# Kernel tuning notes

Measured on AMD Instinct MI355X. Metric: run time of the kernel, lower is better.

The kernel has to match this reference:

```python
import jax, jax.numpy as jnp
import numpy as np
from jax import lax

N = 200; E = 3200; HID = 64; NH = 16; OUT = 2 * HID; CAT = NH * OUT  # CAT = 2048
ALPHA = 0.2


def _gat(h, e_attr, adj, n2n, W, a_s, a_d, a_e, We, concat):
    # edge-feature-aware GAT head: logits from Wh_i, Wh_j and projected node2node feats
    Nn = h.shape[0]
    Wh = h @ W                                       # [N, out]
    ee = ((n2n @ We) @ a_e).reshape(Nn, Nn)          # [N, N] edge-feature term
    logits = jax.nn.leaky_relu((Wh @ a_s)[:, None] + (Wh @ a_d)[None, :] + ee,
                               negative_slope=ALPHA)
    logits = jnp.where(adj > 0, logits, -1e9)        # mask to graph structure
    att = jax.nn.softmax(logits, axis=1)
    h2 = att @ Wh
    if concat:
        h2 = jax.nn.elu(h2)
    return h2, jax.nn.elu(e_attr @ We)               # updated node + edge features


def _edge_pool(x, eidx, e, w, b):
    # static-shape edge pooling: score edges, gate nodes by mean incident score
    src, dst = eidx[0], eidx[1]
    s = jax.nn.sigmoid(jnp.concatenate([x[src], x[dst], e], axis=1) @ w + b)  # [E]
    deg = jax.ops.segment_sum(jnp.ones_like(s), src, num_segments=x.shape[0])
    ns = jax.ops.segment_sum(s, src, num_segments=x.shape[0]) / (deg + 1e-6)
    return x * ns[:, None], e * s[:, None]


def _gpool(x, w, b):
    # GlobalAttention: gate_nn = Linear+Sigmoid, softmax over nodes, weighted sum
    gate = jax.nn.softmax(jax.nn.sigmoid(x @ w + b), axis=0)  # [N, 1]
    return jnp.sum(gate * x, axis=0, keepdims=True)           # [1, D]


def _adj_n2n(Nn, eidx, eattr):
    # vectorized version of the per-edge Python loop in _get_adj_node2node
    src, dst = eidx[0], eidx[1]
    adj = jnp.zeros((Nn, Nn), eattr.dtype).at[src, dst].set(1.0)
    n2n = jnp.zeros((Nn * Nn, eattr.shape[1]), eattr.dtype).at[src * Nn + dst].set(eattr)
    return adj, n2n


def _lstm_dir(x, Wih, Whh, b):
    # one LSTM direction over seq x [T, Din] (PyTorch i,f,g,o gate order)
    Hh = Whh.shape[1]
    def step(carry, xt):
        h, c = carry
        g = xt @ Wih.T + h @ Whh.T + b
        i, f, gg, o = jnp.split(g, 4)
        c = jax.nn.sigmoid(f) * c + jax.nn.sigmoid(i) * jnp.tanh(gg)
        h = jax.nn.sigmoid(o) * jnp.tanh(c)
        return (h, c), h
    (_, _), ys = lax.scan(step, (jnp.zeros(Hh, x.dtype), jnp.zeros(Hh, x.dtype)), x)
    return ys


def setup_inputs():
    key = jax.random.key(0)
    ks = iter(jax.random.split(key, 64))
    def rn(shape, scale=0.05):
        return jax.random.normal(next(ks), shape, jnp.float32) * scale
    inp = {}
    for g in (1, 2):
        eidx = jax.random.randint(next(ks), (2, E), 0, N)
        eattr = rn((E, HID), 1.0)
        adj, n2n = _adj_n2n(N, eidx, eattr)
        inp['features%d' % g] = rn((N, HID), 1.0)
        inp['edge_index%d' % g] = eidx
        inp['edgesAttr%d' % g] = eattr
        inp['adjacency%d' % g] = adj
        inp['node2node%d' % g] = n2n
    inp.update(dict(
        W_h=rn((HID, HID)),
        W_gat=rn((NH, HID, OUT)), a_src=rn((NH, OUT)), a_dst=rn((NH, OUT)),
        a_e=rn((NH, OUT)), We_gat=rn((NH, HID, OUT)),
        W_out=rn((CAT, OUT)), ao_src=rn((OUT,)), ao_dst=rn((OUT,)), ao_e=rn((OUT,)),
        We_out=rn((CAT, OUT)),
        ep1_w=rn((3 * CAT,)), ep1_b=rn(()),
        ep2_w=rn((3 * OUT,)), ep2_b=rn(()),
        g1_w=rn((HID, 1)), g1_b=rn((1,)),
        g2_w=rn((CAT, 1)), g2_b=rn((1,)),
        g3_w=rn((OUT, 1)), g3_b=rn((1,)),
        Wih0=rn((2, 512, 35 * HID)), Whh0=rn((2, 512, 128)), b0=rn((2, 512)),
        Wih1=rn((2, 512, 256)), Whh1=rn((2, 512, 128)), b1=rn((2, 512)),
        fc_w=rn((256, 2)), fc_b=rn((2,)),
    ))
    return inp


def reference(features1, features2, edge_index1, edge_index2, edgesAttr1, edgesAttr2,
              adjacency1, adjacency2, node2node1, node2node2,
              W_h, W_gat, a_src, a_dst, a_e, We_gat,
              W_out, ao_src, ao_dst, ao_e, We_out,
              ep1_w, ep1_b, ep2_w, ep2_b,
              g1_w, g1_b, g2_w, g2_b, g3_w, g3_b,
              Wih0, Whh0, b0, Wih1, Whh1, b1, fc_w, fc_b):
    def graph(feat, eidx, eattr, adj, n2n):
        h = jax.nn.elu(feat @ W_h)                              # SingleNodeAttentionLayer
        hs = [_gpool(h, g1_w, g1_b)]
        outs = [_gat(h, eattr, adj, n2n, W_gat[i], a_src[i], a_dst[i], a_e[i],
                     We_gat[i], True) for i in range(NH)]
        h = jnp.concatenate([o[0] for o in outs], axis=1)       # [N, 2048]
        eattr = jnp.concatenate([o[1] for o in outs], axis=1)   # [E, 2048]
        h, eattr = _edge_pool(h, eidx, eattr, ep1_w, ep1_b)
        hs.append(_gpool(h, g2_w, g2_b))
        adj2, n2n2 = _adj_n2n(h.shape[0], eidx, eattr)          # dense [N*N, 2048]
        h, eattr = _gat(h, eattr, adj2, n2n2, W_out, ao_src, ao_dst, ao_e, We_out, False)
        h, eattr = _edge_pool(h, eidx, eattr, ep2_w, ep2_b)
        hs.append(_gpool(h, g3_w, g3_b))
        return jnp.concatenate(hs, axis=1)                      # [1, 35*HID]

    h1 = graph(features1, edge_index1, edgesAttr1, adjacency1, node2node1)
    h2 = graph(features2, edge_index2, edgesAttr2, adjacency2, node2node2)
    x = jnp.concatenate([h1, h2], axis=0)                       # seq [2, 2240]
    for Wih, Whh, b in ((Wih0, Whh0, b0), (Wih1, Whh1, b1)):
        f = _lstm_dir(x, Wih[0], Whh[0], b[0])
        r = _lstm_dir(x[::-1], Wih[1], Whh[1], b[1])[::-1]
        x = jnp.concatenate([f, r], axis=1)                     # [2, 256]
    logits = x[-1] @ fc_w + fc_b
    return jax.nn.softmax(logits)[None, :]                      # [1, nclass]
```

## Files before the change

kernel.cpp:

```cpp
#include <hip/hip_runtime.h>
#include <math.h>

#define DI static __device__ __forceinline__

DI float eluf(float x){ return x > 0.f ? x : expm1f(x); }
DI float lreluf(float x){ return x > 0.f ? x : 0.2f*x; }
DI float sigmf(float x){ return 1.f/(1.f+expf(-x)); }

typedef unsigned short u16;
typedef unsigned int   u32;
typedef __attribute__((ext_vector_type(8))) short short8_t;
typedef __attribute__((ext_vector_type(4))) float f32x4;

DI u16 bf16rne(float f){
  u32 u = __float_as_uint(f);
  u += 0x7fffu + ((u>>16)&1u);
  return (u16)(u>>16);
}

DI f32x4 bmfma(short8_t a, short8_t b, f32x4 c){
  return __builtin_amdgcn_mfma_f32_16x16x32_bf16(a, b, c, 0, 0, 0);
}

constexpr int N=200, E=3200, HID=64, NH=16, OUTD=128, CAT=2048, SEQD=2240;
// ... 55 lines not shown
  const float *ep1_w, *ep1_b, *ep2_w, *ep2_b;
  const float *g1_w, *g1_b, *g2_w, *g2_b, *g3_w, *g3_b;
  const float *Wih0, *Whh0, *b0, *Wih1, *Whh1, *b1, *fc_w, *fc_b;
  float *out;
};

constexpr int ZPG  = 2*E + 1024;
constexpr int IB_Z = (2*ZPG+255)/256;
constexpr int IB_C = (2*N*N+255)/256;
constexpr int IB_D = (2*2*512*128)/256;
constexpr int IB_E = (NH*HID+CAT+3)/4;
constexpr int IB_H = (2*N+3)/4;
constexpr int IB_W1 = (NH*OUTD*HID)/256;
constexpr int IB_W2 = (OUTD*CAT)/256;
constexpr int IB_EA = (2*E*HID)/256;
__global__ void k_init(Params P){
  int b = blockIdx.x, tid = threadIdx.x;
  if (b < IB_Z){
    int i = b*256 + tid;
    if (i < 2*ZPG){
      int g = i/ZPG, r = i%ZPG;
      int addr = r<E ? OEW1+r : (r<2*E ? OEWV+(r-E) :
                 (r<2*E+512 ? ODEG1+(r-2*E) : ODEG2+(r-2*E-512)));
      gf(g)[addr] = 0.f;
    }
  } else if (b < IB_Z+IB_C){
    int i = (b-IB_Z)*256 + tid; if (i < 2*N*N) G_PIDX[i] = -1;
  } else if (b < IB_Z+IB_C+IB_D){
    int idx = (b-IB_Z-IB_C)*256 + tid;
    int l = idx >> 17;
    int r = idx & 131071;
    int d = r >> 16;
    int r2 = r & 65535;
    int gate = r2 & 511;
    int k = r2 >> 9;
    const float* Whh = l ? P.Whh1 : P.Whh0;
    G_WHHT[idx] = Whh[((size_t)d*512+gate)*128 + k];
  } else if (b < IB_Z+IB_C+IB_D+IB_E){
    int gid = (b-IB_Z-IB_C-IB_D)*4 + (tid>>6);
    int lane = tid & 63;
    if (gid < NH*HID){
      int h = gid/HID, c = gid%HID;
      const float* W = P.We_gat + (size_t)(h*HID+c)*OUTD;
      const float* a = P.a_e + h*OUTD;
      float acc = 0.f;
      for (int o=lane;o<OUTD;o+=64) acc += W[o]*a[o];
      for (int off=32;off>0;off>>=1) acc += __shfl_down(acc,off);
      if (lane==0) gwe_ae()[gid] = acc;
    } else if (gid < NH*HID+CAT){
      int c = gid - NH*HID;
      const float* W = P.We_out + (size_t)c*OUTD;
      float acc = 0.f;
      for (int o=lane;o<OUTD;o+=64) acc += W[o]*P.ao_e[o];
      for (int off=32;off>0;off>>=1) acc += __shfl_down(acc,off);
      if (lane==0) gv_e()[c] = acc;
    }
  } else if (b < IB_Z+IB_C+IB_D+IB_E+IB_H){
    int unit = (b-IB_Z-IB_C-IB_D-IB_E)*4 + (tid>>6);
    if (unit >= 2*N) return;
    int g = unit / N, n = unit % N, c = tid & 63;
    const float* feat = P.g[g].feat;
    float acc = 0.f;
    for (int k=0;k<HID;k++) acc += feat[n*HID+k]*P.W_h[k*HID+c];
    float v = eluf(acc);
    float* f = gf(g);
    f[OH0 + n*HID + c] = v;
    float r = v*P.g1_w[c];
    for (int off=32;off>0;off>>=1) r += __shfl_down(r,off);
    if (c==0) f[ORAW1+n] = r;
  } else if (b < IB_Z+IB_C+IB_D+IB_E+IB_H+IB_W1){
    int i = (b-(IB_Z+IB_C+IB_D+IB_E+IB_H))*256 + tid;
    int h = i>>13, o = (i>>6)&127, c = i&63;
    G_WGAT_T[i] = bf16rne(P.We_gat[(size_t)(h*HID+c)*OUTD + o]);
  } else if (b < IB_Z+IB_C+IB_D+IB_E+IB_H+IB_W1+IB_W2){
    int i = (b-(IB_Z+IB_C+IB_D+IB_E+IB_H+IB_W1))*256 + tid;
    int n = i>>11, q = i&2047;
    G_WOUT_T[i] = bf16rne(P.We_out[(size_t)q*OUTD + n]);
  } else {
    int i = (b-(IB_Z+IB_C+IB_D+IB_E+IB_H+IB_W1+IB_W2))*256 + tid;
    int g = i >= E*HID ? 1 : 0;
    G_EATTR_BF[i] = bf16rne(P.g[g].eattr[i - g*E*HID]);
  }
}

__global__ void k_edoth(Params P){
  int b = blockIdx.x, tid = threadIdx.x;
  int g = b / (E/16);
  int e0 = (b % (E/16)) * 16;
  __shared__ float ea[16][HID+1];
  __shared__ float wa[16][HID+1];
  {
    int row = tid >> 4, c0 = (tid & 15)*4;
    float4 v = *(const float4*)&P.g[g].eattr[(size_t)(e0+row)*HID + c0];
    ea[row][c0]=v.x; ea[row][c0+1]=v.y; ea[row][c0+2]=v.z; ea[row][c0+3]=v.w;
    float4 w = *(const float4*)&gwe_ae()[row*HID + c0];
    wa[row][c0]=w.x; wa[row][c0+1]=w.y; wa[row][c0+2]=w.z; wa[row][c0+3]=w.w;
  }
  __syncthreads();
  int h = tid >> 4, el = tid & 15;
  float acc = 0.f;
  #pragma unroll
  for (int c=0;c<HID;c++) acc += ea[el][c]*wa[h][c];
  G_EDOTH[((size_t)g*NH + h)*E + e0 + el] = acc;
}

__global__ void k_Wh(Params P){
  int n = blockIdx.x, h = blockIdx.y, g = blockIdx.z, o = threadIdx.x;
  float* f = gf(g);
  if (h == NH){
    if (n != 0) return;
    __shared__ float att[N];
    __shared__ float sb[128];
    for (int j = o; j < N; j += 128) att[j] = sigmf(f[ORAW1+j] + P.g1_b[0]);
    __syncthreads();
    float m = -3e38f;
    for (int j = o; j < N; j += 128) m = fmaxf(m, att[j]);
    sb[o] = m; __syncthreads();
    for (int s=64;s>0;s>>=1){ if (o<s) sb[o]=fmaxf(sb[o],sb[o+s]); __syncthreads(); }
    m = sb[0]; __syncthreads();
    float ss = 0.f;
    for (int j = o; j < N; j += 128){ float e = expf(att[j]-m); ss += e; }
    sb[o] = ss; __syncthreads();
    for (int s=64;s>0;s>>=1){ if (o<s) sb[o]+=sb[o+s]; __syncthreads(); }
    float inv = 1.f/sb[0]; __syncthreads();
    for (int j = o; j < N; j += 128) att[j] = expf(att[j]-m)*inv;
    __syncthreads();
    if (o < HID){
      float acc = 0.f;
      for (int j=0;j<N;j++) acc += att[j]*f[OH0 + j*HID + o];
      gxseq()[g*SEQD + o] = acc;
    }
    return;
  }
  __shared__ float hs[HID];
  __shared__ float sred[128], dred[128];
  if (o < HID) hs[o] = f[OH0 + n*HID + o];
  __syncthreads();
  const float* W = P.W_gat + (size_t)h*HID*OUTD + o;
  float acc = 0.f;
  for (int c=0;c<HID;c++) acc += hs[c]*W[(size_t)c*OUTD];
  f[OWH + ((size_t)h*N + n)*OUTD + o] = acc;
  sred[o] = acc*P.a_src[h*OUTD+o];
  dred[o] = acc*P.a_dst[h*OUTD+o];
  __syncthreads();
  for (int s=64;s>0;s>>=1){ if (o<s){ sred[o]+=sred[o+s]; dred[o]+=dred[o+s]; } __syncthreads(); }
  if (o==0){ f[OASN+h*N+n]=sred[0]; f[OADN+h*N+n]=dred[0]; }
}

__global__ void k_att1(Params P){
  int nb = blockIdx.x, h = blockIdx.y, g = blockIdx.z, tid = threadIdx.x;
  int n0 = nb*4;
  __shared__ float z[4][N];
  __shared__ float red[128];
  __shared__ float sinv[4];
  float* f = gf(g);
  const float* adj = P.g[g].adj;
  const int* pidx = gpidx(g);
  const float* edoth = G_EDOTH + ((size_t)g*NH + h)*E;
  const float* adn = f + OADN + h*N;
  for (int i=0;i<4;i++){
    float asn = f[OASN + h*N + n0+i];
    for (int j = tid; j < N; j += 128){
      float a = adj[(n0+i)*N + j];
      float zz;
      if (a > 0.f){
        int p = pidx[(n0+i)*N + j];
        float ee = (p >= 0) ? edoth[p] : 0.f;
        zz = lreluf(asn + adn[j] + ee);
      } else zz = -1e9f;
      z[i][j] = zz;
    }
  }
  __syncthreads();
  for (int i=0;i<4;i++){
    float m = -3e38f;
    for (int j = tid; j < N; j += 128) m = fmaxf(m, z[i][j]);
    red[tid] = m; __syncthreads();
    for (int s=64;s>0;s>>=1){ if (tid<s) red[tid]=fmaxf(red[tid],red[tid+s]); __syncthreads(); }
    m = red[0]; __syncthreads();
    float ssum = 0.f;
    for (int j = tid; j < N; j += 128){ float e = expf(z[i][j]-m); z[i][j]=e; ssum += e; }
    red[tid] = ssum; __syncthreads();
    for (int s=64;s>0;s>>=1){ if (tid<s) red[tid]+=red[tid+s]; __syncthreads(); }
    if (tid==0) sinv[i] = 1.f/red[0];
    __syncthreads();
  }
  const float* wh = f + OWH + (size_t)h*N*OUTD;
  float a0=0.f,a1=0.f,a2=0.f,a3=0.f;
  for (int j=0;j<N;j++){
    float w = wh[(size_t)j*OUTD + tid];
    a0 += z[0][j]*w; a1 += z[1][j]*w; a2 += z[2][j]*w; a3 += z[3][j]*w;
  }
  f[OH1 + (size_t)(n0+0)*CAT + h*OUTD + tid] = eluf(a0*sinv[0]);
  f[OH1 + (size_t)(n0+1)*CAT + h*OUTD + tid] = eluf(a1*sinv[1]);
  f[OH1 + (size_t)(n0+2)*CAT + h*OUTD + tid] = eluf(a2*sinv[2]);
  f[OH1 + (size_t)(n0+3)*CAT + h*OUTD + tid] = eluf(a3*sinv[3]);
}

__global__ void k_xw1(Params P){
  int n = blockIdx.x, g = blockIdx.y, tid = threadIdx.x;
  __shared__ float s1b[256], s2b[256], s3b[256];
  float* f = gf(g);
  const float* x = f + OH1 + (size_t)n*CAT;
  float a1 = 0.f, a2 = 0.f, a3 = 0.f;
  for (int c = tid; c < CAT; c += 256){
    float xv = x[c];
    a1 += xv*P.ep1_w[c];
    a2 += xv*P.ep1_w[CAT+c];
    a3 += xv*P.g2_w[c];
  }
  s1b[tid]=a1; s2b[tid]=a2; s3b[tid]=a3; __syncthreads();
  for (int s=128;s>0;s>>=1){
    if (tid<s){ s1b[tid]+=s1b[tid+s]; s2b[tid]+=s2b[tid+s]; s3b[tid]+=s3b[tid+s]; }
    __syncthreads();
  }
  if (tid==0){ f[OXW1+n]=s1b[0]; f[OXW2+n]=s2b[0]; f[ORAW2+n]=s3b[0]; }
}

__global__ void k_s1(Params P){
  int e = blockIdx.x*256 + threadIdx.x, g = blockIdx.y;
  if (e >= E) return;
  float* f = gf(g);
  const int* ei = P.g[g].eidx;
  int s = ei[e], d = ei[E+e];
  float v = sigmf(f[OXW1+s] + f[OXW2+d] + f[OEW1+e] + P.ep1_b[0]);
  f[OS1+e] = v;
  atomicAdd(&f[OSS1+s], v);
  atomicAdd(&f[ODEG1+s], 1.f);
}

__global__ void k_pairs(Params P){
  int e = blockIdx.x*256 + threadIdx.x, g = blockIdx.y;
  if (e >= E) return;
  const int* ei = P.g[g].eidx;
  atomicMax(&gpidx(g)[ei[e]*N + ei[E+e]], e);
}

__global__ void k_gpool_out(Params P, int xoff, int D, int odeg, int rawoff,
                            const float* b, int outoff){
  int cb = blockIdx.x, g = blockIdx.y, tid = threadIdx.x;
  __shared__ float att[N];
  __shared__ float sb[256];
  float* f = gf(g);
  for (int n = tid; n < N; n += 256){
    float sc = f[odeg+256+n]/(f[odeg+n]+1e-6f);
    att[n] = sigmf(f[rawoff+n]*sc + b[0]);
  }
  __syncthreads();
  float m = -3e38f;
  for (int n = tid; n < N; n += 256) m = fmaxf(m, att[n]);
  sb[tid] = m; __syncthreads();
  for (int s=128;s>0;s>>=1){ if (tid<s) sb[tid]=fmaxf(sb[tid],sb[tid+s]); __syncthreads(); }
  m = sb[0]; __syncthreads();
  float ss = 0.f;
  for (int n = tid; n < N; n += 256){ float e = expf(att[n]-m); ss += e; }
  sb[tid] = ss; __syncthreads();
  for (int s=128;s>0;s>>=1){ if (tid<s) sb[tid]+=sb[tid+s]; __syncthreads(); }
  float inv = 1.f/sb[0]; __syncthreads();
  for (int n = tid; n < N; n += 256){
    float sc = f[odeg+256+n]/(f[odeg+n]+1e-6f);
    att[n] = expf(att[n]-m)*inv*sc;
  }
  __syncthreads();
  int c = cb*256 + tid;
  if (c < D){
    const float* x = f + xoff;
    float acc = 0.f;
    for (int n=0;n<N;n++) acc += att[n]*x[(size_t)n*D + c];
    gxseq()[g*SEQD + outoff + c] = acc;
  }
}

__global__ void k_Wh2(Params P){
  int n = blockIdx.x, g = blockIdx.y, tid = threadIdx.x;
  int kq = tid >> 7, o = tid & 127;
  __shared__ float hrow[4][128];
  __shared__ float part[4][128];
  __shared__ float sr[128], dr[128];
  float* f = gf(g);
  const float* x = f + OH1 + (size_t)n*CAT;
  float acc = 0.f;
  for (int cc=0; cc<4; cc++){
    int c0 = kq*512 + cc*128;
    __syncthreads();
    hrow[kq][o] = x[c0 + o];
    __syncthreads();
    const float* W = P.W_out + (size_t)c0*OUTD + o;
    for (int j=0;j<128;j++) acc += hrow[kq][j]*W[(size_t)j*OUTD];
  }
  part[kq][o] = acc;
  __syncthreads();
  if (kq==0){
    float ns = f[OSS1+n]/(f[ODEG1+n]+1e-6f);
    float a = part[0][o]+part[1][o]+part[2][o]+part[3][o];
    float v = a*ns;
    f[OWH2 + (size_t)n*OUTD + o] = v;
    sr[o] = v*P.ao_src[o];
    dr[o] = v*P.ao_dst[o];
  }
  __syncthreads();
  for (int s=64;s>0;s>>=1){
    if (tid<s){ sr[tid]+=sr[tid+s]; dr[tid]+=dr[tid+s]; }
    __syncthreads();
  }
  if (tid==0){ f[OAS2+n]=sr[0]; f[OAD2+n]=dr[0]; }
}

__global__ void k_att2(Params P){
  int n = blockIdx.x, g = blockIdx.y, tid = threadIdx.x;
  __shared__ float z[N];
  __shared__ float red[128];
  __shared__ float dred[128];
  __shared__ float gred[128];
  float* f = gf(g);
  const float* adj = P.g[g].adj;
  const int* pidx = gpidx(g);
  float asn = f[OAS2+n];
  const float* adn = f + OAD2;
  for (int j = tid; j < N; j += 128){
    float a = adj[n*N + j];
    float zz;
    if (a > 0.f){
      int p = pidx[n*N + j];
      float ee = (p >= 0) ? f[OEWV+p]*f[OS1+p] : 0.f;
      zz = lreluf(asn + adn[j] + ee);
    } else zz = -1e9f;
    z[j] = zz;
  }
  __syncthreads();
  float m = -3e38f;
  for (int j = tid; j < N; j += 128) m = fmaxf(m, z[j]);
  red[tid] = m; __syncthreads();
  for (int s=64;s>0;s>>=1){ if (tid<s) red[tid]=fmaxf(red[tid],red[tid+s]); __syncthreads(); }
  m = red[0]; __syncthreads();
  float ssum = 0.f;
  for (int j = tid; j < N; j += 128){ float e = expf(z[j]-m); z[j]=e; ssum += e; }
  red[tid] = ssum; __syncthreads();
  for (int s=64;s>0;s>>=1){ if (tid<s) red[tid]+=red[tid+s]; __syncthreads(); }
  float inv = 1.f/red[0]; __syncthreads();
  const float* wh = f + OWH2;
  float acc = 0.f;
  for (int j=0;j<N;j++){
    float w = z[j];
    if (w != 0.f) acc += w * wh[(size_t)j*OUTD + tid];
  }
  float v = acc*inv;
  f[OH2B + (size_t)n*OUTD + tid] = v;
  red[tid]  = v*P.ep2_w[tid];
  dred[tid] = v*P.ep2_w[OUTD+tid];
  gred[tid] = v*P.g3_w[tid];
  __syncthreads();
  for (int s=64;s>0;s>>=1){
    if (tid<s){ red[tid]+=red[tid+s]; dred[tid]+=dred[tid+s]; gred[tid]+=gred[tid+s]; }
    __syncthreads();
  }
  if (tid==0){ f[OXS2+n]=red[0]; f[OXD2+n]=dred[0]; f[ORAW3+n]=gred[0]; }
}

__global__ __launch_bounds__(256) void k_e2p_mfma(Params P){
  int eb = blockIdx.x, hg = blockIdx.y, g = blockIdx.z;
  int tid = threadIdx.x;
  int wave = tid>>6, lane = tid&63, l16 = lane&15, l4 = lane>>4;
  __shared__ __attribute__((aligned(16))) u16 Tlds[32*512];
  int e0 = eb*32;
  int nt0 = wave*2;
  const u16* ea = G_EATTR_BF + ((size_t)g*E + e0)*HID;
  short8_t af00 = *(const short8_t*)(ea + l16*HID + l4*8);
  short8_t af01 = *(const short8_t*)(ea + l16*HID + 32 + l4*8);
  short8_t af10 = *(const short8_t*)(ea + (16+l16)*HID + l4*8);
  short8_t af11 = *(const short8_t*)(ea + (16+l16)*HID + 32 + l4*8);
  float ew1p0[4] = {0.f,0.f,0.f,0.f}, ewvp0[4] = {0.f,0.f,0.f,0.f};
  float ew1p1[4] = {0.f,0.f,0.f,0.f}, ewvp1[4] = {0.f,0.f,0.f,0.f};
  for (int hh=0; hh<4; hh++){
    int h = hg*4 + hh;
    const u16* Wg = G_WGAT_T + (size_t)h*OUTD*HID;
    #pragma unroll
    for (int nn=0; nn<2; nn++){
      int nt = nt0 + nn;
      const u16* Wgn = Wg + (size_t)(nt*16 + l16)*HID + l4*8;
      short8_t wg0 = *(const short8_t*)Wgn;
      short8_t wg1 = *(const short8_t*)(Wgn + 32);
      f32x4 d0 = {0.f,0.f,0.f,0.f}, d1 = {0.f,0.f,0.f,0.f};
      d0 = bmfma(af00, wg0, d0);
      d1 = bmfma(af10, wg0, d1);
      d0 = bmfma(af01, wg1, d0);
      d1 = bmfma(af11, wg1, d1);
      int qg = h*OUTD + nt*16 + l16;
      float w1 = P.ep1_w[2*CAT + qg];
      float wv = gv_e()[qg];
      int qloc = hh*128 + nt*16 + l16;
      #pragma unroll
      for (int r=0;r<4;r++){
        float v0 = d0[r] > 0.f ? d0[r] : expm1f(d0[r]);
        float v1 = d1[r] > 0.f ? d1[r] : expm1f(d1[r]);
        ew1p0[r] += v0*w1; ewvp0[r] += v0*wv;
        ew1p1[r] += v1*w1; ewvp1[r] += v1*wv;
        int row = l4*4 + r;
        int byt = (row*1024 + qloc*2) ^ ((row&7)<<4);
        *(u16*)((char*)Tlds + byt) = bf16rne(v0);
        *(u16*)((char*)Tlds + byt + 16384) = bf16rne(v1);
      }
    }
  }
  const u16* WoA = G_WOUT_T + (size_t)(wave*32 + l16)*CAT + hg*512 + l4*8;
  const u16* WoB = WoA + 16*CAT;
  short8_t w0a = *(const short8_t*)WoA;
  short8_t w0b = *(const short8_t*)WoB;
  short8_t w1a = *(const short8_t*)(WoA + 32);
  short8_t w1b = *(const short8_t*)(WoB + 32);
  float* f = gf(g);
  #pragma unroll
  for (int r=0;r<4;r++){
    float a0 = ew1p0[r], b0 = ewvp0[r], a1 = ew1p1[r], b1 = ewvp1[r];
    a0 += __shfl_xor(a0,1); b0 += __shfl_xor(b0,1); a1 += __shfl_xor(a1,1); b1 += __shfl_xor(b1,1);
    a0 += __shfl_xor(a0,2); b0 += __shfl_xor(b0,2); a1 += __shfl_xor(a1,2); b1 += __shfl_xor(b1,2);
    a0 += __shfl_xor(a0,4); b0 += __shfl_xor(b0,4); a1 += __shfl_xor(a1,4); b1 += __shfl_xor(b1,4);
    a0 += __shfl_xor(a0,8); b0 += __shfl_xor(b0,8); a1 += __shfl_xor(a1,8); b1 += __shfl_xor(b1,8);
    if (l16==0){
      int e = e0 + l4*4 + r;
      atomicAdd(&f[OEW1+e], a0);
      atomicAdd(&f[OEWV+e], b0);
      atomicAdd(&f[OEW1+e+16], a1);
      atomicAdd(&f[OEWV+e+16], b1);
    }
  }
  __syncthreads();
  f32x4 acc00 = {0.f,0.f,0.f,0.f}, acc01 = {0.f,0.f,0.f,0.f};
  f32x4 acc10 = {0.f,0.f,0.f,0.f}, acc11 = {0.f,0.f,0.f,0.f};
  #pragma unroll
  for (int ks=0; ks<16; ks++){
    short8_t na = w0a, nb = w0b;
    if (ks < 14){
      na = *(const short8_t*)(WoA + (ks+2)*32);
      nb = *(const short8_t*)(WoB + (ks+2)*32);
    }
    int byt = (l16*1024 + ks*64 + l4*16) ^ ((l16&7)<<4);
    short8_t a0 = *(const short8_t*)((const char*)Tlds + byt);
    short8_t a1 = *(const short8_t*)((const char*)Tlds + byt + 16384);
    acc00 = bmfma(a0, w0a, acc00);
    acc10 = bmfma(a1, w0a, acc10);
    acc01 = bmfma(a0, w0b, acc01);
    acc11 = bmfma(a1, w0b, acc11);
    w0a = w1a; w0b = w1b; w1a = na; w1b = nb;
  }
  float* dst = G_E2PART + (((size_t)hg*2 + g)*E + e0)*OUTD;
  #pragma unroll
  for (int r=0;r<4;r++){
    int ee = l4*4 + r;
    dst[(size_t)ee*OUTD + wave*32 + l16]      = acc00[r];
    dst[(size_t)ee*OUTD + wave*32 + 16 + l16] = acc01[r];
    dst[(size_t)(16+ee)*OUTD + wave*32 + l16]      = acc10[r];
    dst[(size_t)(16+ee)*OUTD + wave*32 + 16 + l16] = acc11[r];
  }
}

constexpr int TE2 = 16;
__global__ void k_ew2fin(Params P){
  int e0 = blockIdx.x*TE2, g = blockIdx.y, tid = threadIdx.x;
  __shared__ float lred[2][TE2];
  float* f = gf(g);
  float w2 = P.ep2_w[2*OUTD + tid];
  int lane = tid & 63, wvi = tid >> 6;
  for (int e=0;e<TE2;e++){
    const float* src = G_E2PART + ((size_t)g*E + e0 + e)*OUTD + tid;
    float a = 0.f;
    for (int h=0;h<4;h++) a += src[(size_t)h*2*E*OUTD];
    float v = eluf(f[OS1+e0+e]*a) * w2;
    for (int off=32;off>0;off>>=1) v += __shfl_down(v,off);
    if (lane==0) lred[wvi][e]=v;
  }
  __syncthreads();
  if (tid < TE2){
    int e = e0 + tid;
    float ew2 = lred[0][tid]+lred[1][tid];
    const int* ei = P.g[g].eidx;
    int s = ei[e], d = ei[E+e];
    float v = sigmf(f[OXS2+s] + f[OXD2+d] + ew2 + P.ep2_b[0]);
    atomicAdd(&f[OSS2+s], v);
    atomicAdd(&f[ODEG2+s], 1.f);
  }
}

__global__ void k_lstm_xg(Params P, int layer){
  int gid = blockIdx.x*4 + (threadIdx.x>>6);
  int lane = threadIdx.x & 63;
  int t = gid >> 10;
  int rem = gid & 1023;
  int d = rem >> 9;
  int gate = rem & 511;
  const float* Wih = layer ? P.Wih1 : P.Wih0;
  const float* bb  = layer ? P.b1   : P.b0;
  const float* xin = layer ? gy0()  : gxseq();
  int Din = layer ? 256 : SEQD;
  const float* x = xin + t*Din;
  const float* Wr = Wih + ((size_t)d*512 + gate)*Din;
  float acc = 0.f;
  for (int k=lane; k<Din; k+=64) acc += x[k]*Wr[k];
  for (int off=32; off>0; off>>=1) acc += __shfl_down(acc, off);
  if (lane==0) gxg()[(t*2 + d)*512 + gate] = acc + bb[d*512 + gate];
}

__global__ void k_lstm_rec(Params P, int layer){
  int d = blockIdx.x, tid = threadIdx.x;
  float* yout = layer ? gy1() : gy0();
  const float* T = G_WHHT + (size_t)(layer*2 + d)*128*512;
  __shared__ float h[128], c[128], gbuf[512];
  if (tid < 128){ h[tid]=0.f; c[tid]=0.f; }
  __syncthreads();
  for (int s=0;s<2;s++){
    int t = (d==0) ? s : 1-s;
    float acc = gxg()[(t*2 + d)*512 + tid];
    for (int k=0;k<128;k++) acc += h[k]*T[(size_t)k*512 + tid];
    gbuf[tid] = acc;
    __syncthreads();
    if (tid < 128){
      float ii = sigmf(gbuf[tid]);
      float ff = sigmf(gbuf[128+tid]);
      float gg = tanhf(gbuf[256+tid]);
      float oo = sigmf(gbuf[384+tid]);
      float cn = ff*c[tid] + ii*gg;
      c[tid] = cn;
      float hn = oo*tanhf(cn);
      h[tid] = hn;
      yout[t*256 + d*128 + tid] = hn;
    }
    __syncthreads();
  }
}

__global__ void k_final(Params P){
  int tid = threadIdx.x;
  __shared__ float sb[256], sb2[256];
  const float* x = gy1() + 256;
  sb[tid]  = x[tid]*P.fc_w[tid*2+0];
  sb2[tid] = x[tid]*P.fc_w[tid*2+1];
  __syncthreads();
  for (int s=128;s>0;s>>=1){ if (tid<s){ sb[tid]+=sb[tid+s]; sb2[tid]+=sb2[tid+s]; } __syncthreads(); }
  if (tid==0){
    float l0 = sb[0] + P.fc_b[0];
    float l1 = sb2[0] + P.fc_b[1];
    float m = fmaxf(l0,l1);
    float e0 = expf(l0-m), e1 = expf(l1-m), inv = 1.f/(e0+e1);
    P.out[0] = e0*inv;
    P.out[1] = e1*inv;
  }
}

extern "C" void kernel_launch(void* const* d_in, const int* in_sizes, int n_in,
                              void* d_out, int out_size, void* d_ws, size_t ws_size,
                              hipStream_t stream){
  Params P;
  for (int g=0; g<2; ++g){
    int b = g*5;
    P.g[g].feat  = (const float*)d_in[b+0];
    P.g[g].eidx  = (const int*)d_in[b+1];
    P.g[g].eattr = (const float*)d_in[b+2];
    P.g[g].adj   = (const float*)d_in[b+3];
    P.g[g].n2n   = (const float*)d_in[b+4];
  }
  P.W_h   = (const float*)d_in[10];
  P.W_gat = (const float*)d_in[11];
  P.a_src = (const float*)d_in[12];
  P.a_dst = (const float*)d_in[13];
  P.a_e   = (const float*)d_in[14];
  P.We_gat= (const float*)d_in[15];
  P.W_out = (const float*)d_in[16];
  P.ao_src= (const float*)d_in[17];
  P.ao_dst= (const float*)d_in[18];
  P.ao_e  = (const float*)d_in[19];
  P.We_out= (const float*)d_in[20];
  P.ep1_w = (const float*)d_in[21];
  P.ep1_b = (const float*)d_in[22];
  P.ep2_w = (const float*)d_in[23];
  P.ep2_b = (const float*)d_in[24];
  P.g1_w  = (const float*)d_in[25];
  P.g1_b  = (const float*)d_in[26];
  P.g2_w  = (const float*)d_in[27];
  P.g2_b  = (const float*)d_in[28];
  P.g3_w  = (const float*)d_in[29];
  P.g3_b  = (const float*)d_in[30];
  P.Wih0  = (const float*)d_in[31];
  P.Whh0  = (const float*)d_in[32];
  P.b0    = (const float*)d_in[33];
  P.Wih1  = (const float*)d_in[34];
  P.Whh1  = (const float*)d_in[35];
  P.b1    = (const float*)d_in[36];
  P.fc_w  = (const float*)d_in[37];
  P.fc_b  = (const float*)d_in[38];
  P.out   = (float*)d_out;

  k_init <<<dim3(IB_Z+IB_C+IB_D+IB_E+IB_H+IB_W1+IB_W2+IB_EA), 256, 0, stream>>>(P);
  k_pairs<<<dim3((E+255)/256,2), 256, 0, stream>>>(P);
  k_edoth<<<dim3(2*(E/16)), 256, 0, stream>>>(P);
  k_e2p_mfma<<<dim3(E/32, 4, 2), 256, 0, stream>>>(P);
  k_Wh   <<<dim3(N,NH+1,2), 128, 0, stream>>>(P);
  k_att1 <<<dim3(N/4,NH,2),128, 0, stream>>>(P);
  k_xw1  <<<dim3(N,2),    256, 0, stream>>>(P);
  k_s1   <<<dim3((E+255)/256,2), 256, 0, stream>>>(P);
  k_gpool_out<<<dim3(8,2), 256, 0, stream>>>(P, OH1, CAT, ODEG1, ORAW2, P.g2_b, HID);
  k_Wh2  <<<dim3(N,2),    512, 0, stream>>>(P);
  k_att2 <<<dim3(N,2),    128, 0, stream>>>(P);
  k_ew2fin<<<dim3(E/TE2,2),128, 0, stream>>>(P);
  k_gpool_out<<<dim3(1,2), 256, 0, stream>>>(P, OH2B, OUTD, ODEG2, ORAW3, P.g3_b, HID+CAT);

  k_lstm_xg <<<dim3(512), 256, 0, stream>>>(P, 0);
  k_lstm_rec<<<dim3(2),   512, 0, stream>>>(P, 0);
  k_lstm_xg <<<dim3(512), 256, 0, stream>>>(P, 1);
  k_lstm_rec<<<dim3(2),   512, 0, stream>>>(P, 1);
  k_final<<<dim3(1), 256, 0, stream>>>(P);
}
```

Before: 367.6 us.

## Merge independent early kernels into one mega-launch and fuse both gpool launches

Combines the pair-index, edge-dot, edge-projection MFMA and Wh kernels into a single launch that dispatches on block index with shared scratch memory. It also merges the two global-attention pooling launches into one 512-thread kernel and moves the first pooling later in the stream. The aim is to cut launch count and let independent work overlap on the GPU. The cost is a single 32KB shared allocation for every block, which may lower occupancy for the lighter bodies. It also relies on k_pairs' atomicMax results being ready before k_att1 runs, which still holds because k_att1 is a later launch.

```diff
diff --git a/kernel.cpp b/kernel.cpp
--- a/kernel.cpp
+++ b/kernel.cpp
@@ -161,286 +161,14 @@
     G_EATTR_BF[i] = bf16rne(P.g[g].eattr[i - g*E*HID]);
   }
 }
-
-__global__ void k_edoth(Params P){
-  int b = blockIdx.x, tid = threadIdx.x;
-  int g = b / (E/16);
-  int e0 = (b % (E/16)) * 16;
-  __shared__ float ea[16][HID+1];
-  __shared__ float wa[16][HID+1];
-  {
-    int row = tid >> 4, c0 = (tid & 15)*4;
-    float4 v = *(const float4*)&P.g[g].eattr[(size_t)(e0+row)*HID + c0];
-    ea[row][c0]=v.x; ea[row][c0+1]=v.y; ea[row][c0+2]=v.z; ea[row][c0+3]=v.w;
-    float4 w = *(const float4*)&gwe_ae()[row*HID + c0];
-    wa[row][c0]=w.x; wa[row][c0+1]=w.y; wa[row][c0+2]=w.z; wa[row][c0+3]=w.w;
-  }
-  __syncthreads();
-  int h = tid >> 4, el = tid & 15;
-  float acc = 0.f;
-  #pragma unroll
-  for (int c=0;c<HID;c++) acc += ea[el][c]*wa[h][c];
-  G_EDOTH[((size_t)g*NH + h)*E + e0 + el] = acc;
-}
-
-__global__ void k_Wh(Params P){
-  int n = blockIdx.x, h = blockIdx.y, g = blockIdx.z, o = threadIdx.x;
-  float* f = gf(g);
-  if (h == NH){
-    if (n != 0) return;
-    __shared__ float att[N];
-    __shared__ float sb[128];
-    for (int j = o; j < N; j += 128) att[j] = sigmf(f[ORAW1+j] + P.g1_b[0]);
-    __syncthreads();
-    float m = -3e38f;
-    for (int j = o; j < N; j += 128) m = fmaxf(m, att[j]);
-    sb[o] = m; __syncthreads();
-    for (int s=64;s>0;s>>=1){ if (o<s) sb[o]=fmaxf(sb[o],sb[o+s]); __syncthreads(); }
-    m = sb[0]; __syncthreads();
-    float ss = 0.f;
-    for (int j = o; j < N; j += 128){ float e = expf(att[j]-m); ss += e; }
-    sb[o] = ss; __syncthreads();
-    for (int s=64;s>0;s>>=1){ if (o<s) sb[o]+=sb[o+s]; __syncthreads(); }
-    float inv = 1.f/sb[0]; __syncthreads();
-    for (int j = o; j < N; j += 128) att[j] = expf(att[j]-m)*inv;
-    __syncthreads();
-    if (o < HID){
-      float acc = 0.f;
-      for (int j=0;j<N;j++) acc += att[j]*f[OH0 + j*HID + o];
-      gxseq()[g*SEQD + o] = acc;
-    }
-    return;
-  }
-  __shared__ float hs[HID];
-  __shared__ float sred[128], dred[128];
-  if (o < HID) hs[o] = f[OH0 + n*HID + o];
-  __syncthreads();
-  const float* W = P.W_gat + (size_t)h*HID*OUTD + o;
-  float acc = 0.f;
-  for (int c=0;c<HID;c++) acc += hs[c]*W[(size_t)c*OUTD];
-  f[OWH + ((size_t)h*N + n)*OUTD + o] = acc;
-  sred[o] = acc*P.a_src[h*OUTD+o];
-  dred[o] = acc*P.a_dst[h*OUTD+o];
-  __syncthreads();
-  for (int s=64;s>0;s>>=1){ if (o<s){ sred[o]+=sred[o+s]; dred[o]+=dred[o+s]; } __syncthreads(); }
-  if (o==0){ f[OASN+h*N+n]=sred[0]; f[OADN+h*N+n]=dred[0]; }
-}
-
-__global__ void k_att1(Params P){
-  int nb = blockIdx.x, h = blockIdx.y, g = blockIdx.z, tid = threadIdx.x;
-  int n0 = nb*4;
-  __shared__ float z[4][N];
-  __shared__ float red[128];
-  __shared__ float sinv[4];
-  float* f = gf(g);
-  const float* adj = P.g[g].adj;
-  const int* pidx = gpidx(g);
-  const float* edoth = G_EDOTH + ((size_t)g*NH + h)*E;
-  const float* adn = f + OADN + h*N;
-  for (int i=0;i<4;i++){
-    float asn = f[OASN + h*N + n0+i];
-    for (int j = tid; j < N; j += 128){
-      float a = adj[(n0+i)*N + j];
-      float zz;
-      if (a > 0.f){
-        int p = pidx[(n0+i)*N + j];
-        float ee = (p >= 0) ? edoth[p] : 0.f;
-        zz = lreluf(asn + adn[j] + ee);
-      } else zz = -1e9f;
-      z[i][j] = zz;
-    }
-  }
-  __syncthreads();
-  for (int i=0;i<4;i++){
-    float m = -3e38f;
-    for (int j = tid; j < N; j += 128) m = fmaxf(m, z[i][j]);
-    red[tid] = m; __syncthreads();
-    for (int s=64;s>0;s>>=1){ if (tid<s) red[tid]=fmaxf(red[tid],red[tid+s]); __syncthreads(); }
-    m = red[0]; __syncthreads();
-    float ssum = 0.f;
-    for (int j = tid; j < N; j += 128){ float e = expf(z[i][j]-m); z[i][j]=e; ssum += e; }
-    red[tid] = ssum; __syncthreads();
-    for (int s=64;s>0;s>>=1){ if (tid<s) red[tid]+=red[tid+s]; __syncthreads(); }
-    if (tid==0) sinv[i] = 1.f/red[0];
-    __syncthreads();
-  }
-  const float* wh = f + OWH + (size_t)h*N*OUTD;
-  float a0=0.f,a1=0.f,a2=0.f,a3=0.f;
-  for (int j=0;j<N;j++){
-    float w = wh[(size_t)j*OUTD + tid];
-    a0 += z[0][j]*w; a1 += z[1][j]*w; a2 += z[2][j]*w; a3 += z[3][j]*w;
-  }
-  f[OH1 + (size_t)(n0+0)*CAT + h*OUTD + tid] = eluf(a0*sinv[0]);
-  f[OH1 + (size_t)(n0+1)*CAT + h*OUTD + tid] = eluf(a1*sinv[1]);
-  f[OH1 + (size_t)(n0+2)*CAT + h*OUTD + tid] = eluf(a2*sinv[2]);
-  f[OH1 + (size_t)(n0+3)*CAT + h*OUTD + tid] = eluf(a3*sinv[3]);
-}
-
-__global__ void k_xw1(Params P){
-  int n = blockIdx.x, g = blockIdx.y, tid = threadIdx.x;
-  __shared__ float s1b[256], s2b[256], s3b[256];
-  float* f = gf(g);
-  const float* x = f + OH1 + (size_t)n*CAT;
-  float a1 = 0.f, a2 = 0.f, a3 = 0.f;
-  for (int c = tid; c < CAT; c += 256){
-    float xv = x[c];
-    a1 += xv*P.ep1_w[c];
-    a2 += xv*P.ep1_w[CAT+c];
-    a3 += xv*P.g2_w[c];
-  }
-  s1b[tid]=a1; s2b[tid]=a2; s3b[tid]=a3; __syncthreads();
-  for (int s=128;s>0;s>>=1){
-    if (tid<s){ s1b[tid]+=s1b[tid+s]; s2b[tid]+=s2b[tid+s]; s3b[tid]+=s3b[tid+s]; }
-    __syncthreads();
-  }
-  if (tid==0){ f[OXW1+n]=s1b[0]; f[OXW2+n]=s2b[0]; f[ORAW2+n]=s3b[0]; }
-}
-
-__global__ void k_s1(Params P){
-  int e = blockIdx.x*256 + threadIdx.x, g = blockIdx.y;
-  if (e >= E) return;
-  float* f = gf(g);
-  const int* ei = P.g[g].eidx;
-  int s = ei[e], d = ei[E+e];
-  float v = sigmf(f[OXW1+s] + f[OXW2+d] + f[OEW1+e] + P.ep1_b[0]);
-  f[OS1+e] = v;
-  atomicAdd(&f[OSS1+s], v);
-  atomicAdd(&f[ODEG1+s], 1.f);
-}
-
-__global__ void k_pairs(Params P){
-  int e = blockIdx.x*256 + threadIdx.x, g = blockIdx.y;
-  if (e >= E) return;
-  const int* ei = P.g[g].eidx;
-  atomicMax(&gpidx(g)[ei[e]*N + ei[E+e]], e);
-}
-
-__global__ void k_gpool_out(Params P, int xoff, int D, int odeg, int rawoff,
-                            const float* b, int outoff){
-  int cb = blockIdx.x, g = blockIdx.y, tid = threadIdx.x;
-  __shared__ float att[N];
-  __shared__ float sb[256];
-  float* f = gf(g);
-  for (int n = tid; n < N; n += 256){
-    float sc = f[odeg+256+n]/(f[odeg+n]+1e-6f);
-    att[n] = sigmf(f[rawoff+n]*sc + b[0]);
-  }
-  __syncthreads();
-  float m = -3e38f;
-  for (int n = tid; n < N; n += 256) m = fmaxf(m, att[n]);
-  sb[tid] = m; __syncthreads();
-  for (int s=128;s>0;s>>=1){ if (tid<s) sb[tid]=fmaxf(sb[tid],sb[tid+s]); __syncthreads(); }
-  m = sb[0]; __syncthreads();
-  float ss = 0.f;
-  for (int n = tid; n < N; n += 256){ float e = expf(att[n]-m); ss += e; }
-  sb[tid] = ss; __syncthreads();
-  for (int s=128;s>0;s>>=1){ if (tid<s) sb[tid]+=sb[tid+s]; __syncthreads(); }
-  float inv = 1.f/sb[0]; __syncthreads();
-  for (int n = tid; n < N; n += 256){
-    float sc = f[odeg+256+n]/(f[odeg+n]+1e-6f);
-    att[n] = expf(att[n]-m)*inv*sc;
-  }
-  __syncthreads();
-  int c = cb*256 + tid;
-  if (c < D){
-    const float* x = f + xoff;
-    float acc = 0.f;
-    for (int n=0;n<N;n++) acc += att[n]*x[(size_t)n*D + c];
-    gxseq()[g*SEQD + outoff + c] = acc;
-  }
-}
-
-__global__ void k_Wh2(Params P){
-  int n = blockIdx.x, g = blockIdx.y, tid = threadIdx.x;
-  int kq = tid >> 7, o = tid & 127;
-  __shared__ float hrow[4][128];
-  __shared__ float part[4][128];
-  __shared__ float sr[128], dr[128];
-  float* f = gf(g);
-  const float* x = f + OH1 + (size_t)n*CAT;
-  float acc = 0.f;
-  for (int cc=0; cc<4; cc++){
-    int c0 = kq*512 + cc*128;
-    __syncthreads();
-    hrow[kq][o] = x[c0 + o];
-    __syncthreads();
-    const float* W = P.W_out + (size_t)c0*OUTD + o;
-    for (int j=0;j<128;j++) acc += hrow[kq][j]*W[(size_t)j*OUTD];
-  }
-  part[kq][o] = acc;
-  __syncthreads();
-  if (kq==0){
-    float ns = f[OSS1+n]/(f[ODEG1+n]+1e-6f);
-    float a = part[0][o]+part[1][o]+part[2][o]+part[3][o];
-    float v = a*ns;
-    f[OWH2 + (size_t)n*OUTD + o] = v;
-    sr[o] = v*P.ao_src[o];
-    dr[o] = v*P.ao_dst[o];
-  }
-  __syncthreads();
-  for (int s=64;s>0;s>>=1){
-    if (tid<s){ sr[tid]+=sr[tid+s]; dr[tid]+=dr[tid+s]; }
-    __syncthreads();
-  }
-  if (tid==0){ f[OAS2+n]=sr[0]; f[OAD2+n]=dr[0]; }
-}
-
-__global__ void k_att2(Params P){
-  int n = blockIdx.x, g = blockIdx.y, tid = threadIdx.x;
-  __shared__ float z[N];
-  __shared__ float red[128];
-  __shared__ float dred[128];
-  __shared__ float gred[128];
-  float* f = gf(g);
-  const float* adj = P.g[g].adj;
-  const int* pidx = gpidx(g);
-  float asn = f[OAS2+n];
-  const float* adn = f + OAD2;
-  for (int j = tid; j < N; j += 128){
-    float a = adj[n*N + j];
-    float zz;
-    if (a > 0.f){
-      int p = pidx[n*N + j];
-      float ee = (p >= 0) ? f[OEWV+p]*f[OS1+p] : 0.f;
-      zz = lreluf(asn + adn[j] + ee);
-    } else zz = -1e9f;
-    z[j] = zz;
-  }
-  __syncthreads();
-  float m = -3e38f;
-  for (int j = tid; j < N; j += 128) m = fmaxf(m, z[j]);
-  red[tid] = m; __syncthreads();
-  for (int s=64;s>0;s>>=1){ if (tid<s) red[tid]=fmaxf(red[tid],red[tid+s]); __syncthreads(); }
-  m = red[0]; __syncthreads();
-  float ssum = 0.f;
-  for (int j = tid; j < N; j += 128){ float e = expf(z[j]-m); z[j]=e; ssum += e; }
-  red[tid] = ssum; __syncthreads();
-  for (int s=64;s>0;s>>=1){ if (tid<s) red[tid]+=red[tid+s]; __syncthreads(); }
-  float inv = 1.f/red[0]; __syncthreads();
-  const float* wh = f + OWH2;
-  float acc = 0.f;
-  for (int j=0;j<N;j++){
-    float w = z[j];
-    if (w != 0.f) acc += w * wh[(size_t)j*OUTD + tid];
-  }
-  float v = acc*inv;
-  f[OH2B + (size_t)n*OUTD + tid] = v;
-  red[tid]  = v*P.ep2_w[tid];
-  dred[tid] = v*P.ep2_w[OUTD+tid];
-  gred[tid] = v*P.g3_w[tid];
-  __syncthreads();
-  for (int s=64;s>0;s>>=1){
-    if (tid<s){ red[tid]+=red[tid+s]; dred[tid]+=dred[tid+s]; gred[tid]+=gred[tid+s]; }
-    __syncthreads();
-  }
-  if (tid==0){ f[OXS2+n]=red[0]; f[OXD2+n]=dred[0]; f[ORAW3+n]=gred[0]; }
-}
-
-__global__ __launch_bounds__(256) void k_e2p_mfma(Params P){
-  int eb = blockIdx.x, hg = blockIdx.y, g = blockIdx.z;
+constexpr int IB_TOT = IB_Z+IB_C+IB_D+IB_E+IB_H+IB_W1+IB_W2+IB_EA;
+
+
+DI void e2p_body(Params& P, int idx, char* smem){
+  int g = idx/400, r2 = idx%400, hg = r2/100, eb = r2%100;
   int tid = threadIdx.x;
   int wave = tid>>6, lane = tid&63, l16 = lane&15, l4 = lane>>4;
-  __shared__ __attribute__((aligned(16))) u16 Tlds[32*512];
+  u16* Tlds = (u16*)smem;
   int e0 = eb*32;
   int nt0 = wave*2;
   const u16* ea = G_EATTR_BF + ((size_t)g*E + e0)*HID;
@@ -533,6 +261,306 @@
   }
 }
 
+DI void edoth_body(Params& P, int idx, float* s){
+  int tid = threadIdx.x;
+  int g = idx / (E/16);
+  int e0 = (idx % (E/16)) * 16;
+  float (*ea)[HID+1] = (float(*)[HID+1])s;
+  float (*wa)[HID+1] = (float(*)[HID+1])(s + 16*(HID+1));
+  {
+    int row = tid >> 4, c0 = (tid & 15)*4;
+    float4 v = *(const float4*)&P.g[g].eattr[(size_t)(e0+row)*HID + c0];
+    ea[row][c0]=v.x; ea[row][c0+1]=v.y; ea[row][c0+2]=v.z; ea[row][c0+3]=v.w;
+    float4 w = *(const float4*)&gwe_ae()[row*HID + c0];
+    wa[row][c0]=w.x; wa[row][c0+1]=w.y; wa[row][c0+2]=w.z; wa[row][c0+3]=w.w;
+  }
+  __syncthreads();
+  int h = tid >> 4, el = tid & 15;
+  float acc = 0.f;
+  #pragma unroll
+  for (int c=0;c<HID;c++) acc += ea[el][c]*wa[h][c];
+  G_EDOTH[((size_t)g*NH + h)*E + e0 + el] = acc;
+}
+
+DI void wh_body(Params& P, int idx, float* s){
+  int o = threadIdx.x;
+  if (o >= 128) return;
+  int g = idx / (N*(NH+1));
+  int r = idx % (N*(NH+1));
+  int h = r / N, n = r % N;
+  float* f = gf(g);
+  if (h == NH){
+    if (n != 0) return;
+    float* att = s;
+    float* sb  = s + 200;
+    for (int j = o; j < N; j += 128) att[j] = sigmf(f[ORAW1+j] + P.g1_b[0]);
+    __syncthreads();
+    float m = -3e38f;
+    for (int j = o; j < N; j += 128) m = fmaxf(m, att[j]);
+    sb[o] = m; __syncthreads();
+    for (int sft=64;sft>0;sft>>=1){ if (o<sft) sb[o]=fmaxf(sb[o],sb[o+sft]); __syncthreads(); }
+    m = sb[0]; __syncthreads();
+    float ss = 0.f;
+    for (int j = o; j < N; j += 128){ float e = expf(att[j]-m); ss += e; }
+    sb[o] = ss; __syncthreads();
+    for (int sft=64;sft>0;sft>>=1){ if (o<sft) sb[o]+=sb[o+sft]; __syncthreads(); }
+    float inv = 1.f/sb[0]; __syncthreads();
+    for (int j = o; j < N; j += 128) att[j] = expf(att[j]-m)*inv;
+    __syncthreads();
+    if (o < HID){
+      float acc = 0.f;
+      for (int j=0;j<N;j++) acc += att[j]*f[OH0 + j*HID + o];
+      gxseq()[g*SEQD + o] = acc;
+    }
+    return;
+  }
+  float* hs   = s;
+  float* sred = s + 64;
+  float* dred = s + 192;
+  if (o < HID) hs[o] = f[OH0 + n*HID + o];
+  __syncthreads();
+  const float* W = P.W_gat + (size_t)h*HID*OUTD + o;
+  float acc = 0.f;
+  for (int c=0;c<HID;c++) acc += hs[c]*W[(size_t)c*OUTD];
+  f[OWH + ((size_t)h*N + n)*OUTD + o] = acc;
+  sred[o] = acc*P.a_src[h*OUTD+o];
+  dred[o] = acc*P.a_dst[h*OUTD+o];
+  __syncthreads();
+  for (int sft=64;sft>0;sft>>=1){ if (o<sft){ sred[o]+=sred[o+sft]; dred[o]+=dred[o+sft]; } __syncthreads(); }
+  if (o==0){ f[OASN+h*N+n]=sred[0]; f[OADN+h*N+n]=dred[0]; }
+}
+
+DI void pairs_body(Params& P, int idx){
+  int g = idx / 13;
+  int e = (idx % 13)*256 + threadIdx.x;
+  if (e >= E) return;
+  const int* ei = P.g[g].eidx;
+  atomicMax(&gpidx(g)[ei[e]*N + ei[E+e]], e);
+}
+
+constexpr int MB_E2P = 800, MB_ED = 400, MB_WH = 2*N*(NH+1), MB_PR = 26;
+__global__ __launch_bounds__(256) void k_mega(Params P){
+  __shared__ __attribute__((aligned(16))) char smem[32768];
+  int b = blockIdx.x;
+  if (b < MB_E2P) e2p_body(P, b, smem);
+  else if (b < MB_E2P+MB_ED) edoth_body(P, b-MB_E2P, (float*)smem);
+  else if (b < MB_E2P+MB_ED+MB_WH) wh_body(P, b-(MB_E2P+MB_ED), (float*)smem);
+  else pairs_body(P, b-(MB_E2P+MB_ED+MB_WH));
+}
+
+__global__ void k_att1(Params P){
+  int nb = blockIdx.x, h = blockIdx.y, g = blockIdx.z, tid = threadIdx.x;
+  int n0 = nb*4;
+  __shared__ float z[4][N];
+  __shared__ float red[128];
+  __shared__ float sinv[4];
+  float* f = gf(g);
+  const float* adj = P.g[g].adj;
+  const int* pidx = gpidx(g);
+  const float* edoth = G_EDOTH + ((size_t)g*NH + h)*E;
+  const float* adn = f + OADN + h*N;
+  for (int i=0;i<4;i++){
+    float asn = f[OASN + h*N + n0+i];
+    for (int j = tid; j < N; j += 128){
+      float a = adj[(n0+i)*N + j];
+      float zz;
+      if (a > 0.f){
+        int p = pidx[(n0+i)*N + j];
+        float ee = (p >= 0) ? edoth[p] : 0.f;
+        zz = lreluf(asn + adn[j] + ee);
+      } else zz = -1e9f;
+      z[i][j] = zz;
+    }
+  }
+  __syncthreads();
+  for (int i=0;i<4;i++){
+    float m = -3e38f;
+    for (int j = tid; j < N; j += 128) m = fmaxf(m, z[i][j]);
+    red[tid] = m; __syncthreads();
+    for (int s=64;s>0;s>>=1){ if (tid<s) red[tid]=fmaxf(red[tid],red[tid+s]); __syncthreads(); }
+    m = red[0]; __syncthreads();
+    float ssum = 0.f;
+    for (int j = tid; j < N; j += 128){ float e = expf(z[i][j]-m); z[i][j]=e; ssum += e; }
+    red[tid] = ssum; __syncthreads();
+    for (int s=64;s>0;s>>=1){ if (tid<s) red[tid]+=red[tid+s]; __syncthreads(); }
+    if (tid==0) sinv[i] = 1.f/red[0];
+    __syncthreads();
+  }
+  const float* wh = f + OWH + (size_t)h*N*OUTD;
+  float a0=0.f,a1=0.f,a2=0.f,a3=0.f;
+  for (int j=0;j<N;j++){
+    float w = wh[(size_t)j*OUTD + tid];
+    a0 += z[0][j]*w; a1 += z[1][j]*w; a2 += z[2][j]*w; a3 += z[3][j]*w;
+  }
+  f[OH1 + (size_t)(n0+0)*CAT + h*OUTD + tid] = eluf(a0*sinv[0]);
+  f[OH1 + (size_t)(n0+1)*CAT + h*OUTD + tid] = eluf(a1*sinv[1]);
+  f[OH1 + (size_t)(n0+2)*CAT + h*OUTD + tid] = eluf(a2*sinv[2]);
+  f[OH1 + (size_t)(n0+3)*CAT + h*OUTD + tid] = eluf(a3*sinv[3]);
+}
+
+__global__ void k_xw1(Params P){
+  int n = blockIdx.x, g = blockIdx.y, tid = threadIdx.x;
+  __shared__ float s1b[256], s2b[256], s3b[256];
+  float* f = gf(g);
+  const float* x = f + OH1 + (size_t)n*CAT;
+  float a1 = 0.f, a2 = 0.f, a3 = 0.f;
+  for (int c = tid; c < CAT; c += 256){
+    float xv = x[c];
+    a1 += xv*P.ep1_w[c];
+    a2 += xv*P.ep1_w[CAT+c];
+    a3 += xv*P.g2_w[c];
+  }
+  s1b[tid]=a1; s2b[tid]=a2; s3b[tid]=a3; __syncthreads();
+  for (int s=128;s>0;s>>=1){
+    if (tid<s){ s1b[tid]+=s1b[tid+s]; s2b[tid]+=s2b[tid+s]; s3b[tid]+=s3b[tid+s]; }
+    __syncthreads();
+  }
+  if (tid==0){ f[OXW1+n]=s1b[0]; f[OXW2+n]=s2b[0]; f[ORAW2+n]=s3b[0]; }
+}
+
+__global__ void k_s1(Params P){
+  int e = blockIdx.x*256 + threadIdx.x, g = blockIdx.y;
+  if (e >= E) return;
+  float* f = gf(g);
+  const int* ei = P.g[g].eidx;
+  int s = ei[e], d = ei[E+e];
+  float v = sigmf(f[OXW1+s] + f[OXW2+d] + f[OEW1+e] + P.ep1_b[0]);
+  f[OS1+e] = v;
+  atomicAdd(&f[OSS1+s], v);
+  atomicAdd(&f[ODEG1+s], 1.f);
+}
+
+DI void gpool_body(Params& P, int xoff, int D, int odeg, int rawoff,
+                   const float* bb, int outoff, int cb, int g,
+                   float* att, float* sb){
+  int tid = threadIdx.x;
+  float* f = gf(g);
+  if (tid < N){
+    float sc = f[odeg+256+tid]/(f[odeg+tid]+1e-6f);
+    att[tid] = sigmf(f[rawoff+tid]*sc + bb[0]);
+  }
+  __syncthreads();
+  float m = (tid < N) ? att[tid] : -3e38f;
+  sb[tid] = m; __syncthreads();
+  for (int s=256;s>0;s>>=1){ if (tid<s) sb[tid]=fmaxf(sb[tid],sb[tid+s]); __syncthreads(); }
+  m = sb[0]; __syncthreads();
+  float e = (tid < N) ? expf(att[tid]-m) : 0.f;
+  sb[tid] = e; __syncthreads();
+  for (int s=256;s>0;s>>=1){ if (tid<s) sb[tid]+=sb[tid+s]; __syncthreads(); }
+  float inv = 1.f/sb[0]; __syncthreads();
+  if (tid < N){
+    float sc = f[odeg+256+tid]/(f[odeg+tid]+1e-6f);
+    att[tid] = e*inv*sc;
+  }
+  __syncthreads();
+  int c = cb*512 + tid;
+  if (c < D){
+    const float* x = f + xoff;
+    float acc = 0.f;
+    for (int n=0;n<N;n++) acc += att[n]*x[(size_t)n*D + c];
+    gxseq()[g*SEQD + outoff + c] = acc;
+  }
+}
+
+__global__ void k_gpools(Params P){
+  __shared__ float att[N];
+  __shared__ float sb[512];
+  int b = blockIdx.x;
+  if (b < 8){
+    int g = b >> 2, cb = b & 3;
+    gpool_body(P, OH1, CAT, ODEG1, ORAW2, P.g2_b, HID, cb, g, att, sb);
+  } else {
+    int g = b - 8;
+    gpool_body(P, OH2B, OUTD, ODEG2, ORAW3, P.g3_b, HID+CAT, 0, g, att, sb);
+  }
+}
+
+__global__ void k_Wh2(Params P){
+  int n = blockIdx.x, g = blockIdx.y, tid = threadIdx.x;
+  int kq = tid >> 7, o = tid & 127;
+  __shared__ float hrow[4][128];
+  __shared__ float part[4][128];
+  __shared__ float sr[128], dr[128];
+  float* f = gf(g);
+  const float* x = f + OH1 + (size_t)n*CAT;
+  float acc = 0.f;
+  for (int cc=0; cc<4; cc++){
+    int c0 = kq*512 + cc*128;
+    __syncthreads();
+    hrow[kq][o] = x[c0 + o];
+    __syncthreads();
+    const float* W = P.W_out + (size_t)c0*OUTD + o;
+    for (int j=0;j<128;j++) acc += hrow[kq][j]*W[(size_t)j*OUTD];
+  }
+  part[kq][o] = acc;
+  __syncthreads();
+  if (kq==0){
+    float ns = f[OSS1+n]/(f[ODEG1+n]+1e-6f);
+    float a = part[0][o]+part[1][o]+part[2][o]+part[3][o];
+    float v = a*ns;
+    f[OWH2 + (size_t)n*OUTD + o] = v;
+    sr[o] = v*P.ao_src[o];
+    dr[o] = v*P.ao_dst[o];
+  }
+  __syncthreads();
+  for (int s=64;s>0;s>>=1){
+    if (tid<s){ sr[tid]+=sr[tid+s]; dr[tid]+=dr[tid+s]; }
+    __syncthreads();
+  }
+  if (tid==0){ f[OAS2+n]=sr[0]; f[OAD2+n]=dr[0]; }
+}
+
+__global__ void k_att2(Params P){
+  int n = blockIdx.x, g = blockIdx.y, tid = threadIdx.x;
+  __shared__ float z[N];
+  __shared__ float red[128];
+  __shared__ float dred[128];
+  __shared__ float gred[128];
+  float* f = gf(g);
+  const float* adj = P.g[g].adj;
+  const int* pidx = gpidx(g);
+  float asn = f[OAS2+n];
+  const float* adn = f + OAD2;
+  for (int j = tid; j < N; j += 128){
+    float a = adj[n*N + j];
+    float zz;
+    if (a > 0.f){
+      int p = pidx[n*N + j];
+      float ee = (p >= 0) ? f[OEWV+p]*f[OS1+p] : 0.f;
+      zz = lreluf(asn + adn[j] + ee);
+    } else zz = -1e9f;
+    z[j] = zz;
+  }
+  __syncthreads();
+  float m = -3e38f;
+  for (int j = tid; j < N; j += 128) m = fmaxf(m, z[j]);
+  red[tid] = m; __syncthreads();
+  for (int s=64;s>0;s>>=1){ if (tid<s) red[tid]=fmaxf(red[tid],red[tid+s]); __syncthreads(); }
+  m = red[0]; __syncthreads();
+  float ssum = 0.f;
+  for (int j = tid; j < N; j += 128){ float e = expf(z[j]-m); z[j]=e; ssum += e; }
+  red[tid] = ssum; __syncthreads();
+  for (int s=64;s>0;s>>=1){ if (tid<s) red[tid]+=red[tid+s]; __syncthreads(); }
+  float inv = 1.f/red[0]; __syncthreads();
+  const float* wh = f + OWH2;
+  float acc = 0.f;
+  for (int j=0;j<N;j++){
+    float w = z[j];
+    if (w != 0.f) acc += w * wh[(size_t)j*OUTD + tid];
+  }
+  float v = acc*inv;
+  f[OH2B + (size_t)n*OUTD + tid] = v;
+  red[tid]  = v*P.ep2_w[tid];
+  dred[tid] = v*P.ep2_w[OUTD+tid];
+  gred[tid] = v*P.g3_w[tid];
+  __syncthreads();
+  for (int s=64;s>0;s>>=1){
+    if (tid<s){ red[tid]+=red[tid+s]; dred[tid]+=dred[tid+s]; gred[tid]+=gred[tid+s]; }
+    __syncthreads();
+  }
+  if (tid==0){ f[OXS2+n]=red[0]; f[OXD2+n]=dred[0]; f[ORAW3+n]=gred[0]; }
+}
+
 constexpr int TE2 = 16;
 __global__ void k_ew2fin(Params P){
   int e0 = blockIdx.x*TE2, g = blockIdx.y, tid = threadIdx.x;
@@ -543,6 +571,7 @@
   for (int e=0;e<TE2;e++){
     const float* src = G_E2PART + ((size_t)g*E + e0 + e)*OUTD + tid;
     float a = 0.f;
+    #pragma unroll
     for (int h=0;h<4;h++) a += src[(size_t)h*2*E*OUTD];
     float v = eluf(f[OS1+e0+e]*a) * w2;
     for (int off=32;off>0;off>>=1) v += __shfl_down(v,off);
@@ -668,19 +697,15 @@
   P.fc_b  = (const float*)d_in[38];
   P.out   = (float*)d_out;
 
-  k_init <<<dim3(IB_Z+IB_C+IB_D+IB_E+IB_H+IB_W1+IB_W2+IB_EA), 256, 0, stream>>>(P);
-  k_pairs<<<dim3((E+255)/256,2), 256, 0, stream>>>(P);
-  k_edoth<<<dim3(2*(E/16)), 256, 0, stream>>>(P);
-  k_e2p_mfma<<<dim3(E/32, 4, 2), 256, 0, stream>>>(P);
-  k_Wh   <<<dim3(N,NH+1,2), 128, 0, stream>>>(P);
+  k_init <<<dim3(IB_TOT), 256, 0, stream>>>(P);
+  k_mega <<<dim3(MB_E2P+MB_ED+MB_WH+MB_PR), 256, 0, stream>>>(P);
   k_att1 <<<dim3(N/4,NH,2),128, 0, stream>>>(P);
   k_xw1  <<<dim3(N,2),    256, 0, stream>>>(P);
   k_s1   <<<dim3((E+255)/256,2), 256, 0, stream>>>(P);
-  k_gpool_out<<<dim3(8,2), 256, 0, stream>>>(P, OH1, CAT, ODEG1, ORAW2, P.g2_b, HID);
   k_Wh2  <<<dim3(N,2),    512, 0, stream>>>(P);
   k_att2 <<<dim3(N,2),    128, 0, stream>>>(P);
   k_ew2fin<<<dim3(E/TE2,2),128, 0, stream>>>(P);
-  k_gpool_out<<<dim3(1,2), 256, 0, stream>>>(P, OH2B, OUTD, ODEG2, ORAW3, P.g3_b, HID+CAT);
+  k_gpools<<<dim3(10),    512, 0, stream>>>(P);
 
   k_lstm_xg <<<dim3(512), 256, 0, stream>>>(P, 0);
   k_lstm_rec<<<dim3(2),   512, 0, stream>>>(P, 0);
```

After: 338.3 us. 1.09x faster.
